# Optimization experiments

Hardware: AMD Instinct MI355X
Metric: run time of the kernel (lower is better)

Reference implementation:

```python
import jax, jax.numpy as jnp
import numpy as np

B, N, IN_F = 8, 1024, 512
H, D = 4, 128  # num_heads, out_features; H*D == IN_F for residual
LN_EPS = 1e-5
NEG_INF = -1e9


def setup_inputs() -> dict:
    key = jax.random.key(0)
    ks = jax.random.split(key, 7)
    x = jax.random.normal(ks[0], (B, N, IN_F), dtype=jnp.float32)
    mask = jax.random.randint(ks[1], (B, N), 0, 2, dtype=jnp.int32)
    # xavier-uniform-ish init scales
    W = jax.random.uniform(ks[2], (IN_F, H * D), dtype=jnp.float32, minval=-1.0, maxval=1.0) * (1.414 * np.sqrt(6.0 / (IN_F + H * D)))
    a_src = jax.random.uniform(ks[3], (H, D), dtype=jnp.float32, minval=-1.0, maxval=1.0) * (1.414 * np.sqrt(6.0 / (H + D)))
    a_dst = jax.random.uniform(ks[4], (H, D), dtype=jnp.float32, minval=-1.0, maxval=1.0) * (1.414 * np.sqrt(6.0 / (H + D)))
    gamma = jnp.ones((H * D,), dtype=jnp.float32)
    beta = jnp.zeros((H * D,), dtype=jnp.float32)
    return {"x": x, "mask": mask, "W": W, "a_src": a_src, "a_dst": a_dst, "gamma": gamma, "beta": beta}


def _layernorm(y, gamma, beta):
    mu = jnp.mean(y, axis=-1, keepdims=True)
    var = jnp.var(y, axis=-1, keepdims=True)
    return (y - mu) * jax.lax.rsqrt(var + LN_EPS) * gamma + beta


def reference(x, mask, W, a_src, a_dst, gamma, beta):
    b, n, _ = x.shape
    h = (x @ W).reshape(b, n, H, D)                      # [B,N,H,D]
    e_i = jnp.einsum('bnhd,hd->bnh', h, a_src)           # [B,N,H]
    e_j = jnp.einsum('bnhd,hd->bnh', h, a_dst)           # [B,N,H]
    e = jax.nn.leaky_relu(e_i[:, :, None, :] + e_j[:, None, :, :], 0.2)  # [B,N,N,H]
    mm = mask[:, None, :, None] * mask[:, :, None, None]  # [B,N,N,1]
    e = jnp.where(mm == 0, NEG_INF, e)
    attn = jax.nn.softmax(e, axis=2)                     # softmax over neighbors j
    h_prime = jnp.einsum('bnjh,bjhd->bnhd', attn, h).reshape(b, n, H * D)
    return _layernorm(h_prime + x, gamma, beta)
```

## Files before the change

### kernel.cpp

```cpp
#include <hip/hip_runtime.h>
#include <math.h>

#define Bsz 8
#define Nn 1024
#define Ff 512
#define Hh 4
#define Dd 128

typedef float f32x4 __attribute__((ext_vector_type(4)));
typedef short bf16x8 __attribute__((ext_vector_type(8)));

#define LOG2E 1.44269504f

__device__ inline uint f2b1(float a) {
    union { float f; uint u; } v; v.f = a;
    return (v.u + 0x7fffu + ((v.u >> 16) & 1u)) >> 16;
}
__device__ inline uint f2b_pk(float a, float b) { return f2b1(a) | (f2b1(b) << 16); }


__global__ __launch_bounds__(256) void conv_w(const float* __restrict__ Wm,
                                              ushort* __restrict__ Wc) {
    __shared__ float tile[8 * 520];
    const int kb = blockIdx.x, tid = threadIdx.x;
    const int l = tid & 63, wv = tid >> 6;
    const int col0 = l * 8;
    #pragma unroll
    for (int rsel = 0; rsel < 2; ++rsel) {
        int kr = wv + rsel * 4;
        const float4* wp = (const float4*)(Wm + (size_t)(kb * 8 + kr) * Ff + col0);
        float4 a = wp[0], c = wp[1];
        *(float4*)(&tile[kr * 520 + col0]) = a;
        *(float4*)(&tile[kr * 520 + col0 + 4]) = c;
    }
    __syncthreads();
    #pragma unroll
    for (int rsel = 0; rsel < 2; ++rsel) {
        int n = tid + rsel * 256;
        float v[8];
        #pragma unroll
        for (int u = 0; u < 8; ++u) v[u] = tile[u * 520 + n];
        uint4 o = { f2b_pk(v[0], v[1]), f2b_pk(v[2], v[3]),
                    f2b_pk(v[4], v[5]), f2b_pk(v[6], v[7]) };
        int nc = n >> 7, nt = (n >> 4) & 7, n15 = n & 15;
        *(uint4*)(Wc + ((size_t)(((nc * 64 + kb) * 8 + nt) * 16 + n15) << 3)) = o;
    }
}

__global__ __launch_bounds__(256, 2) void gemm_xw(const float* __restrict__ X,
                                                  const ushort* __restrict__ Wc,
                                                  const float* __restrict__ a_src,
                                                  const float* __restrict__ a_dst,
                                                  ushort* __restrict__ hT,
                                                  float* __restrict__ ei,
                                                  float* __restrict__ ej) {
    __shared__ ushort Bs[2][4096];
    const int idx = blockIdx.x;
    const int b = idx & 7, sub = idx >> 3;
    const int mi = sub & 15, nc = sub >> 4;
    const int tid = threadIdx.x;
    const int w = tid >> 6, lane = tid & 63, quad = lane >> 4, l16 = lane & 15;
    const int mtile = (b * 16 + mi) * 4 + w;

    f32x4 z = {0.f, 0.f, 0.f, 0.f};
    f32x4 acc[8];
    #pragma unroll
    for (int nt = 0; nt < 8; ++nt) acc[nt] = z;

    const float* ap = X + (size_t)(mtile * 16 + l16) * Ff + quad * 8;
    const ushort* wsrc = Wc + ((size_t)nc << 16) + tid * 16;
    const int brd = quad * 1024 + l16 * 8;

#define LOADA(s, dst) { \
        float4 f0_ = *(const float4*)(ap + (s) * 32); \
        float4 f1_ = *(const float4*)(ap + (s) * 32 + 4); \
        union { uint4 u; bf16x8 v; } o_; \
        o_.u.x = f2b_pk(f0_.x, f0_.y); o_.u.y = f2b_pk(f0_.z, f0_.w); \
        o_.u.z = f2b_pk(f1_.x, f1_.y); o_.u.w = f2b_pk(f1_.z, f1_.w); \
        dst = o_.v; }

    bf16x8 ab[2];
    bf16x8 br0, br1;

    LOADA(0, ab[0]);
    LOADA(1, ab[1]);
    br0 = *(const bf16x8*)(wsrc);
    br1 = *(const bf16x8*)(wsrc + 8);
    *(bf16x8*)(&Bs[0][tid * 16]) = br0;
    *(bf16x8*)(&Bs[0][tid * 16 + 8]) = br1;
    __syncthreads();

    #pragma unroll 2
    for (int s = 0; s < 16; ++s) {
        const int c = s & 1;
        if (s + 1 < 16) {
            br0 = *(const bf16x8*)(wsrc + (s + 1) * 4096);
            br1 = *(const bf16x8*)(wsrc + (s + 1) * 4096 + 8);
        }
        #pragma unroll
        for (int nt = 0; nt < 8; ++nt) {
            bf16x8 bf = *(const bf16x8*)(&Bs[c][brd + nt * 128]);
            acc[nt] = __builtin_amdgcn_mfma_f32_16x16x32_bf16(ab[c], bf, acc[nt], 0, 0, 0);
        }
        if (s + 2 < 16) LOADA(s + 2, ab[c]);
        if (s + 1 < 16) {
            *(bf16x8*)(&Bs[(s + 1) & 1][tid * 16]) = br0;
            *(bf16x8*)(&Bs[(s + 1) & 1][tid * 16 + 8]) = br1;
        }
        __syncthreads();
    }
#undef LOADA

    const int nseq = (mi * 4 + w) * 16 + quad * 4;
    const int jb = nseq >> 5, js = nseq & 31;
    #pragma unroll
    for (int nt = 0; nt < 8; ++nt) {
        uint2 pv;
        pv.x = f2b_pk(acc[nt][0], acc[nt][1]);
        pv.y = f2b_pk(acc[nt][2], acc[nt][3]);
        int hd = nc * 128 + nt * 16 + l16;
        *(uint2*)(hT + ((size_t)(b * 32 + jb)) * 16384 + (size_t)hd * 32 + js) = pv;
    }

    {
        float as4[8], ad4[8];
        #pragma unroll
        for (int nt = 0; nt < 8; ++nt) {
            as4[nt] = a_src[nc * 128 + nt * 16 + l16] * LOG2E;
            ad4[nt] = a_dst[nc * 128 + nt * 16 + l16] * LOG2E;
        }
        #pragma unroll
        for (int rr = 0; rr < 4; ++rr) {
            float v1 = 0.f, v2 = 0.f;
            #pragma unroll
            for (int nt = 0; nt < 8; ++nt) {
                v1 += acc[nt][rr] * as4[nt];
                v2 += acc[nt][rr] * ad4[nt];
            }
            #pragma unroll
            for (int off = 1; off < 16; off <<= 1) {
                v1 += __shfl_xor(v1, off);
                v2 += __shfl_xor(v2, off);
            }
            if (l16 == 0) {
                int n = nseq + rr;
                ei[((b * 4 + nc) << 10) + n] = v1;
                ej[((b * 4 + nc) << 10) + n] = v2;
            }
        }
    }
}

__global__ __launch_bounds__(512, 2) void attn_pv(const ushort* __restrict__ hT,
                                                  const float* __restrict__ ei_g,
                                                  const float* __restrict__ ej_g,
                                                  const int* __restrict__ mask,
                                                  const float* __restrict__ X,
                                                  const float* __restrict__ gamma,
                                                  const float* __restrict__ beta,
                                                  float* __restrict__ out) {
    __shared__ float s_ep[16 * 516];
    __shared__ float s_as[4][16];

    const int idx = blockIdx.x;
    const int b = idx & 7, i0 = (idx >> 3) * 16;
    const int tid = threadIdx.x;
    const int w = tid >> 6, w4 = w & 3, jh = w >> 2;
    const int lane = tid & 63, quad = lane >> 4, l16 = lane & 15;

    const float* ejh = ej_g + ((b * 4 + w4) << 10);
    const int* mkb = mask + (b << 10);

    float maxej = -3.0e38f;
    #pragma unroll
    for (int k = 0; k < 16; ++k) maxej = fmaxf(maxej, ejh[lane + 64 * k]);
    #pragma unroll
    for (int off = 1; off < 64; off <<= 1) maxej = fmaxf(maxej, __shfl_xor(maxej, off));

    const float ei0 = ei_g[((b * 4 + w4) << 10) + i0 + l16];
    const int mi0 = mkb[i0 + l16];
    float m0;
    { float t = ei0 + maxej; m0 = mi0 ? fmaxf(t, 0.2f * t) : -1e9f; }

    f32x4 z = {0.f, 0.f, 0.f, 0.f};
    f32x4 acc[8], asum = z;
    #pragma unroll
    for (int dt = 0; dt < 8; ++dt) acc[dt] = z;
    bf16x8 ones;
    #pragma unroll
    for (int q = 0; q < 8; ++q) ones[q] = (short)0x3F80;

    const ushort* hTb = hT + ((size_t)(b * 32)) * 16384 + (size_t)(w4 * 128) * 32
                        + l16 * 32 + quad * 8;

    bf16x8 B[2][8];
    #pragma unroll
    for (int c = 0; c < 2; ++c) {
        const ushort* h0 = hTb + (size_t)(jh * 16 + c) * 16384;
        #pragma unroll
        for (int dt = 0; dt < 8; ++dt) B[c][dt] = *(const bf16x8*)(h0 + dt * 512);
    }

    #pragma unroll 2
    for (int r = 0; r < 16; ++r) {
        const int c = r & 1;
        const int jq = (jh * 16 + r) * 32 + quad * 8;
        float4 e0 = *(const float4*)(ejh + jq);
        float4 e1 = *(const float4*)(ejh + jq + 4);
        int4 q0 = *(const int4*)(mkb + jq);
        int4 q1 = *(const int4*)(mkb + jq + 4);
        float ev[8] = {e0.x, e0.y, e0.z, e0.w, e1.x, e1.y, e1.z, e1.w};
        int   mv[8] = {q0.x, q0.y, q0.z, q0.w, q1.x, q1.y, q1.z, q1.w};
        float wv0[8];
        #pragma unroll
        for (int u = 0; u < 8; ++u) {
            float t0 = ei0 + ev[u];
            float l0 = fmaxf(t0, 0.2f * t0);
            wv0[u] = __builtin_amdgcn_exp2f(((mi0 && mv[u]) ? l0 : -1e9f) - m0);
        }
        union { uint4 u; bf16x8 v; } af0;
        af0.u.x = f2b_pk(wv0[0], wv0[1]); af0.u.y = f2b_pk(wv0[2], wv0[3]);
        af0.u.z = f2b_pk(wv0[4], wv0[5]); af0.u.w = f2b_pk(wv0[6], wv0[7]);
        asum = __builtin_amdgcn_mfma_f32_16x16x32_bf16(af0.v, ones, asum, 0, 0, 0);
        #pragma unroll
        for (int dt = 0; dt < 8; ++dt)
            acc[dt] = __builtin_amdgcn_mfma_f32_16x16x32_bf16(af0.v, B[c][dt], acc[dt], 0, 0, 0);
        if (r + 2 < 16) {
            const ushort* hn = hTb + (size_t)(jh * 16 + r + 2) * 16384;
            #pragma unroll
            for (int dt = 0; dt < 8; ++dt) B[c][dt] = *(const bf16x8*)(hn + dt * 512);
        }
    }

    if (jh == 1) {
        #pragma unroll
        for (int dt = 0; dt < 8; ++dt)
            #pragma unroll
            for (int rr = 0; rr < 4; ++rr)
                s_ep[(quad * 4 + rr) * 516 + w4 * 128 + dt * 16 + l16] = acc[dt][rr];
        if (l16 == 0) {
            #pragma unroll
            for (int rr = 0; rr < 4; ++rr)
                s_as[w4][quad * 4 + rr] = asum[rr];
        }
    }
    __syncthreads();
    if (jh == 0) {
        float rs[4];
        #pragma unroll
        for (int rr = 0; rr < 4; ++rr)
            rs[rr] = 1.f / (asum[rr] + s_as[w4][quad * 4 + rr]);
        #pragma unroll
        for (int dt = 0; dt < 8; ++dt)
            #pragma unroll
            for (int rr = 0; rr < 4; ++rr) {
                int off = (quad * 4 + rr) * 516 + w4 * 128 + dt * 16 + l16;
                s_ep[off] = (acc[dt][rr] + s_ep[off]) * rs[rr];
            }
    }
    __syncthreads();

    #pragma unroll
    for (int q = 0; q < 2; ++q) {
        int ir = w * 2 + q;
        int ig = i0 + ir;
        float4 p0 = *(const float4*)(&s_ep[ir * 516 + lane * 8]);
        float4 p1 = *(const float4*)(&s_ep[ir * 516 + lane * 8 + 4]);
        const float* xp = X + (((size_t)((b << 10) + ig)) << 9) + lane * 8;
        float4 x0 = *(const float4*)(xp);
        float4 x1 = *(const float4*)(xp + 4);
        float v[8] = {p0.x + x0.x, p0.y + x0.y, p0.z + x0.z, p0.w + x0.w,
                      p1.x + x1.x, p1.y + x1.y, p1.z + x1.z, p1.w + x1.w};
        float s1 = 0.f, s2 = 0.f;
        #pragma unroll
        for (int u = 0; u < 8; ++u) { s1 += v[u]; s2 += v[u] * v[u]; }
        #pragma unroll
        for (int off = 1; off < 64; off <<= 1) { s1 += __shfl_xor(s1, off); s2 += __shfl_xor(s2, off); }
        float mean = s1 * (1.f / 512.f);
        float var  = s2 * (1.f / 512.f) - mean * mean;
        float rstd = rsqrtf(var + 1e-5f);
        int f0i = lane * 8;
        float4 g0 = *(const float4*)(gamma + f0i);
        float4 g1 = *(const float4*)(gamma + f0i + 4);
        float4 be0 = *(const float4*)(beta + f0i);
        float4 be1 = *(const float4*)(beta + f0i + 4);
        float* op = out + (((size_t)((b << 10) + ig)) << 9) + f0i;
        float4 o0, o1;
        o0.x = (v[0] - mean) * rstd * g0.x + be0.x;
        o0.y = (v[1] - mean) * rstd * g0.y + be0.y;
        o0.z = (v[2] - mean) * rstd * g0.z + be0.z;
        o0.w = (v[3] - mean) * rstd * g0.w + be0.w;
        o1.x = (v[4] - mean) * rstd * g1.x + be1.x;
        o1.y = (v[5] - mean) * rstd * g1.y + be1.y;
        o1.z = (v[6] - mean) * rstd * g1.z + be1.z;
        o1.w = (v[7] - mean) * rstd * g1.w + be1.w;
        *(float4*)op = o0;
        *(float4*)(op + 4) = o1;
    }
}

extern "C" void kernel_launch(void* const* d_in, const int* in_sizes, int n_in,
                              void* d_out, int out_size, void* d_ws, size_t ws_size,
                              hipStream_t stream) {
    const float* x     = (const float*)d_in[0];
    const int*   mask  = (const int*)d_in[1];
    const float* W     = (const float*)d_in[2];
    const float* a_src = (const float*)d_in[3];
    const float* a_dst = (const float*)d_in[4];
    const float* gamma = (const float*)d_in[5];
    const float* beta  = (const float*)d_in[6];
    float* out = (float*)d_out;

    ushort* hT = (ushort*)d_ws;
    ushort* Wc = hT + (size_t)8 * 512 * 1024;
    float* ei = (float*)(Wc + (size_t)512 * 512);
    float* ej = ei + 32768;

    conv_w<<<dim3(64), 256, 0, stream>>>(W, Wc);
    gemm_xw<<<dim3(512), 256, 0, stream>>>(x, Wc, a_src, a_dst, hT, ei, ej);
    attn_pv<<<dim3(512), 512, 0, stream>>>(hT, ei, ej, mask, x, gamma, beta, out);
}
```

Measured before the change: 139.7 us.

## Process 32 query rows per attention block and fully unroll inner loops

The attention kernel now handles two 16-row query tiles per block, so each loaded hT B-fragment feeds twice as many MFMAs. The grid drops from 512 to 256 blocks. The GEMM and attention main loops are also manually unrolled with macros to remove dynamic register-array indexing. The cost is roughly double the accumulator registers and twice the shared memory per block, which may lower occupancy under launch_bounds(512,2) and leaves fewer blocks to fill the CUs.

```diff
diff --git a/kernel.cpp b/kernel.cpp
--- a/kernel.cpp
+++ b/kernel.cpp
@@ -79,36 +79,44 @@
         o_.u.z = f2b_pk(f1_.x, f1_.y); o_.u.w = f2b_pk(f1_.z, f1_.w); \
         dst = o_.v; }
 
-    bf16x8 ab[2];
+    bf16x8 ab0, ab1;
     bf16x8 br0, br1;
 
-    LOADA(0, ab[0]);
-    LOADA(1, ab[1]);
+    LOADA(0, ab0);
+    LOADA(1, ab1);
     br0 = *(const bf16x8*)(wsrc);
     br1 = *(const bf16x8*)(wsrc + 8);
     *(bf16x8*)(&Bs[0][tid * 16]) = br0;
     *(bf16x8*)(&Bs[0][tid * 16 + 8]) = br1;
     __syncthreads();
 
-    #pragma unroll 2
-    for (int s = 0; s < 16; ++s) {
-        const int c = s & 1;
-        if (s + 1 < 16) {
-            br0 = *(const bf16x8*)(wsrc + (s + 1) * 4096);
-            br1 = *(const bf16x8*)(wsrc + (s + 1) * 4096 + 8);
-        }
-        #pragma unroll
-        for (int nt = 0; nt < 8; ++nt) {
-            bf16x8 bf = *(const bf16x8*)(&Bs[c][brd + nt * 128]);
-            acc[nt] = __builtin_amdgcn_mfma_f32_16x16x32_bf16(ab[c], bf, acc[nt], 0, 0, 0);
-        }
-        if (s + 2 < 16) LOADA(s + 2, ab[c]);
-        if (s + 1 < 16) {
-            *(bf16x8*)(&Bs[(s + 1) & 1][tid * 16]) = br0;
-            *(bf16x8*)(&Bs[(s + 1) & 1][tid * 16 + 8]) = br1;
-        }
-        __syncthreads();
-    }
+#define GEMM_STEP(S, ABc) { \
+    if ((S) + 1 < 16) { \
+        br0 = *(const bf16x8*)(wsrc + ((S) + 1) * 4096); \
+        br1 = *(const bf16x8*)(wsrc + ((S) + 1) * 4096 + 8); \
+    } \
+    _Pragma("unroll") \
+    for (int nt = 0; nt < 8; ++nt) { \
+        bf16x8 bf = *(const bf16x8*)(&Bs[(S) & 1][brd + nt * 128]); \
+        acc[nt] = __builtin_amdgcn_mfma_f32_16x16x32_bf16(ABc, bf, acc[nt], 0, 0, 0); \
+    } \
+    if ((S) + 2 < 16) LOADA((S) + 2, ABc); \
+    if ((S) + 1 < 16) { \
+        *(bf16x8*)(&Bs[((S) + 1) & 1][tid * 16]) = br0; \
+        *(bf16x8*)(&Bs[((S) + 1) & 1][tid * 16 + 8]) = br1; \
+    } \
+    __syncthreads(); \
+}
+
+    GEMM_STEP(0, ab0)   GEMM_STEP(1, ab1)
+    GEMM_STEP(2, ab0)   GEMM_STEP(3, ab1)
+    GEMM_STEP(4, ab0)   GEMM_STEP(5, ab1)
+    GEMM_STEP(6, ab0)   GEMM_STEP(7, ab1)
+    GEMM_STEP(8, ab0)   GEMM_STEP(9, ab1)
+    GEMM_STEP(10, ab0)  GEMM_STEP(11, ab1)
+    GEMM_STEP(12, ab0)  GEMM_STEP(13, ab1)
+    GEMM_STEP(14, ab0)  GEMM_STEP(15, ab1)
+#undef GEMM_STEP
 #undef LOADA
 
     const int nseq = (mi * 4 + w) * 16 + quad * 4;
@@ -159,11 +167,11 @@
                                                   const float* __restrict__ gamma,
                                                   const float* __restrict__ beta,
                                                   float* __restrict__ out) {
-    __shared__ float s_ep[16 * 516];
-    __shared__ float s_as[4][16];
+    __shared__ float s_ep[32 * 516];
+    __shared__ float s_as[4][32];
 
     const int idx = blockIdx.x;
-    const int b = idx & 7, i0 = (idx >> 3) * 16;
+    const int b = idx & 7, i0 = (idx >> 3) * 32;
     const int tid = threadIdx.x;
     const int w = tid >> 6, w4 = w & 3, jh = w >> 2;
     const int lane = tid & 63, quad = lane >> 4, l16 = lane & 15;
@@ -178,14 +186,17 @@
     for (int off = 1; off < 64; off <<= 1) maxej = fmaxf(maxej, __shfl_xor(maxej, off));
 
     const float ei0 = ei_g[((b * 4 + w4) << 10) + i0 + l16];
+    const float ei1 = ei_g[((b * 4 + w4) << 10) + i0 + 16 + l16];
     const int mi0 = mkb[i0 + l16];
-    float m0;
+    const int mi1 = mkb[i0 + 16 + l16];
+    float m0, m1;
     { float t = ei0 + maxej; m0 = mi0 ? fmaxf(t, 0.2f * t) : -1e9f; }
+    { float t = ei1 + maxej; m1 = mi1 ? fmaxf(t, 0.2f * t) : -1e9f; }
 
     f32x4 z = {0.f, 0.f, 0.f, 0.f};
-    f32x4 acc[8], asum = z;
-    #pragma unroll
-    for (int dt = 0; dt < 8; ++dt) acc[dt] = z;
+    f32x4 acc0[8], acc1[8], asum0 = z, asum1 = z;
+    #pragma unroll
+    for (int dt = 0; dt < 8; ++dt) { acc0[dt] = z; acc1[dt] = z; }
     bf16x8 ones;
     #pragma unroll
     for (int q = 0; q < 8; ++q) ones[q] = (short)0x3F80;
@@ -193,76 +204,102 @@
     const ushort* hTb = hT + ((size_t)(b * 32)) * 16384 + (size_t)(w4 * 128) * 32
                         + l16 * 32 + quad * 8;
 
-    bf16x8 B[2][8];
-    #pragma unroll
-    for (int c = 0; c < 2; ++c) {
-        const ushort* h0 = hTb + (size_t)(jh * 16 + c) * 16384;
-        #pragma unroll
-        for (int dt = 0; dt < 8; ++dt) B[c][dt] = *(const bf16x8*)(h0 + dt * 512);
-    }
-
-    #pragma unroll 2
-    for (int r = 0; r < 16; ++r) {
-        const int c = r & 1;
-        const int jq = (jh * 16 + r) * 32 + quad * 8;
-        float4 e0 = *(const float4*)(ejh + jq);
-        float4 e1 = *(const float4*)(ejh + jq + 4);
-        int4 q0 = *(const int4*)(mkb + jq);
-        int4 q1 = *(const int4*)(mkb + jq + 4);
-        float ev[8] = {e0.x, e0.y, e0.z, e0.w, e1.x, e1.y, e1.z, e1.w};
-        int   mv[8] = {q0.x, q0.y, q0.z, q0.w, q1.x, q1.y, q1.z, q1.w};
-        float wv0[8];
-        #pragma unroll
-        for (int u = 0; u < 8; ++u) {
-            float t0 = ei0 + ev[u];
-            float l0 = fmaxf(t0, 0.2f * t0);
-            wv0[u] = __builtin_amdgcn_exp2f(((mi0 && mv[u]) ? l0 : -1e9f) - m0);
-        }
-        union { uint4 u; bf16x8 v; } af0;
-        af0.u.x = f2b_pk(wv0[0], wv0[1]); af0.u.y = f2b_pk(wv0[2], wv0[3]);
-        af0.u.z = f2b_pk(wv0[4], wv0[5]); af0.u.w = f2b_pk(wv0[6], wv0[7]);
-        asum = __builtin_amdgcn_mfma_f32_16x16x32_bf16(af0.v, ones, asum, 0, 0, 0);
+    bf16x8 B0[8], B1[8];
+    {
+        const ushort* h0 = hTb + (size_t)(jh * 16 + 0) * 16384;
+        #pragma unroll
+        for (int dt = 0; dt < 8; ++dt) B0[dt] = *(const bf16x8*)(h0 + dt * 512);
+        const ushort* h1 = hTb + (size_t)(jh * 16 + 1) * 16384;
+        #pragma unroll
+        for (int dt = 0; dt < 8; ++dt) B1[dt] = *(const bf16x8*)(h1 + dt * 512);
+    }
+
+#define ATTN_STEP(R, BC) { \
+    const int jq = (jh * 16 + (R)) * 32 + quad * 8; \
+    float4 e0 = *(const float4*)(ejh + jq); \
+    float4 e1 = *(const float4*)(ejh + jq + 4); \
+    int4 q0 = *(const int4*)(mkb + jq); \
+    int4 q1 = *(const int4*)(mkb + jq + 4); \
+    float ev[8] = {e0.x, e0.y, e0.z, e0.w, e1.x, e1.y, e1.z, e1.w}; \
+    int   mv[8] = {q0.x, q0.y, q0.z, q0.w, q1.x, q1.y, q1.z, q1.w}; \
+    float wv0[8], wv1[8]; \
+    _Pragma("unroll") \
+    for (int u = 0; u < 8; ++u) { \
+        float t0 = ei0 + ev[u]; \
+        float l0 = fmaxf(t0, 0.2f * t0); \
+        wv0[u] = __builtin_amdgcn_exp2f(((mi0 && mv[u]) ? l0 : -1e9f) - m0); \
+        float t1 = ei1 + ev[u]; \
+        float l1 = fmaxf(t1, 0.2f * t1); \
+        wv1[u] = __builtin_amdgcn_exp2f(((mi1 && mv[u]) ? l1 : -1e9f) - m1); \
+    } \
+    union { uint4 u; bf16x8 v; } af0, af1; \
+    af0.u.x = f2b_pk(wv0[0], wv0[1]); af0.u.y = f2b_pk(wv0[2], wv0[3]); \
+    af0.u.z = f2b_pk(wv0[4], wv0[5]); af0.u.w = f2b_pk(wv0[6], wv0[7]); \
+    af1.u.x = f2b_pk(wv1[0], wv1[1]); af1.u.y = f2b_pk(wv1[2], wv1[3]); \
+    af1.u.z = f2b_pk(wv1[4], wv1[5]); af1.u.w = f2b_pk(wv1[6], wv1[7]); \
+    asum0 = __builtin_amdgcn_mfma_f32_16x16x32_bf16(af0.v, ones, asum0, 0, 0, 0); \
+    asum1 = __builtin_amdgcn_mfma_f32_16x16x32_bf16(af1.v, ones, asum1, 0, 0, 0); \
+    _Pragma("unroll") \
+    for (int dt = 0; dt < 8; ++dt) { \
+        acc0[dt] = __builtin_amdgcn_mfma_f32_16x16x32_bf16(af0.v, BC[dt], acc0[dt], 0, 0, 0); \
+        acc1[dt] = __builtin_amdgcn_mfma_f32_16x16x32_bf16(af1.v, BC[dt], acc1[dt], 0, 0, 0); \
+    } \
+    if ((R) + 2 < 16) { \
+        const ushort* hn = hTb + (size_t)(jh * 16 + (R) + 2) * 16384; \
+        _Pragma("unroll") \
+        for (int dt = 0; dt < 8; ++dt) BC[dt] = *(const bf16x8*)(hn + dt * 512); \
+    } \
+}
+
+    ATTN_STEP(0, B0)   ATTN_STEP(1, B1)
+    ATTN_STEP(2, B0)   ATTN_STEP(3, B1)
+    ATTN_STEP(4, B0)   ATTN_STEP(5, B1)
+    ATTN_STEP(6, B0)   ATTN_STEP(7, B1)
+    ATTN_STEP(8, B0)   ATTN_STEP(9, B1)
+    ATTN_STEP(10, B0)  ATTN_STEP(11, B1)
+    ATTN_STEP(12, B0)  ATTN_STEP(13, B1)
+    ATTN_STEP(14, B0)  ATTN_STEP(15, B1)
+#undef ATTN_STEP
+
+    if (jh == 1) {
         #pragma unroll
         for (int dt = 0; dt < 8; ++dt)
-            acc[dt] = __builtin_amdgcn_mfma_f32_16x16x32_bf16(af0.v, B[c][dt], acc[dt], 0, 0, 0);
-        if (r + 2 < 16) {
-            const ushort* hn = hTb + (size_t)(jh * 16 + r + 2) * 16384;
-            #pragma unroll
-            for (int dt = 0; dt < 8; ++dt) B[c][dt] = *(const bf16x8*)(hn + dt * 512);
-        }
-    }
-
-    if (jh == 1) {
-        #pragma unroll
-        for (int dt = 0; dt < 8; ++dt)
-            #pragma unroll
-            for (int rr = 0; rr < 4; ++rr)
-                s_ep[(quad * 4 + rr) * 516 + w4 * 128 + dt * 16 + l16] = acc[dt][rr];
+            #pragma unroll
+            for (int rr = 0; rr < 4; ++rr) {
+                s_ep[(quad * 4 + rr) * 516 + w4 * 128 + dt * 16 + l16] = acc0[dt][rr];
+                s_ep[(16 + quad * 4 + rr) * 516 + w4 * 128 + dt * 16 + l16] = acc1[dt][rr];
+            }
         if (l16 == 0) {
             #pragma unroll
-            for (int rr = 0; rr < 4; ++rr)
-                s_as[w4][quad * 4 + rr] = asum[rr];
+            for (int rr = 0; rr < 4; ++rr) {
+                s_as[w4][quad * 4 + rr] = asum0[rr];
+                s_as[w4][16 + quad * 4 + rr] = asum1[rr];
+            }
         }
     }
     __syncthreads();
     if (jh == 0) {
-        float rs[4];
-        #pragma unroll
-        for (int rr = 0; rr < 4; ++rr)
-            rs[rr] = 1.f / (asum[rr] + s_as[w4][quad * 4 + rr]);
+        float rs0[4], rs1[4];
+        #pragma unroll
+        for (int rr = 0; rr < 4; ++rr) {
+            rs0[rr] = 1.f / (asum0[rr] + s_as[w4][quad * 4 + rr]);
+            rs1[rr] = 1.f / (asum1[rr] + s_as[w4][16 + quad * 4 + rr]);
+        }
         #pragma unroll
         for (int dt = 0; dt < 8; ++dt)
             #pragma unroll
             for (int rr = 0; rr < 4; ++rr) {
-                int off = (quad * 4 + rr) * 516 + w4 * 128 + dt * 16 + l16;
-                s_ep[off] = (acc[dt][rr] + s_ep[off]) * rs[rr];
+                int off0 = (quad * 4 + rr) * 516 + w4 * 128 + dt * 16 + l16;
+                s_ep[off0] = (acc0[dt][rr] + s_ep[off0]) * rs0[rr];
+                int off1 = (16 + quad * 4 + rr) * 516 + w4 * 128 + dt * 16 + l16;
+                s_ep[off1] = (acc1[dt][rr] + s_ep[off1]) * rs1[rr];
             }
     }
     __syncthreads();
 
     #pragma unroll
-    for (int q = 0; q < 2; ++q) {
-        int ir = w * 2 + q;
+    for (int q = 0; q < 4; ++q) {
+        int ir = w * 4 + q;
         int ig = i0 + ir;
         float4 p0 = *(const float4*)(&s_ep[ir * 516 + lane * 8]);
         float4 p1 = *(const float4*)(&s_ep[ir * 516 + lane * 8 + 4]);
@@ -318,5 +355,5 @@
 
     conv_w<<<dim3(64), 256, 0, stream>>>(W, Wc);
     gemm_xw<<<dim3(512), 256, 0, stream>>>(x, Wc, a_src, a_dst, hT, ei, ej);
-    attn_pv<<<dim3(512), 512, 0, stream>>>(hT, ei, ej, mask, x, gamma, beta, out);
-}
+    attn_pv<<<dim3(256), 512, 0, stream>>>(hT, ei, ej, mask, x, gamma, beta, out);
+}
```

After: 126.3 us. 1.11x faster.
